# Kernel tuning notes

Hardware: AMD Instinct MI355X
Metric: run time of the kernel (lower is better)

## Reference

```python
import jax, jax.numpy as jnp
import numpy as np

B, C0, N, K = 8, 3, 2048, 20
EMB = 1024
NUM_CLASS = 40
EPS = 1e-5
SLOPE = 0.2


def setup_inputs() -> dict:
    key = jax.random.key(0)
    ks = jax.random.split(key, 16)
    rn = lambda k, s: jax.random.normal(k, s, jnp.float32) * 0.05
    inp = {
        'x': jax.random.normal(ks[0], (B, C0, N), jnp.float32),
        # 1x1 conv weights (out_ch, in_ch)
        'w1': rn(ks[1], (64, 6)),
        'w2': rn(ks[2], (64, 128)),
        'w3': rn(ks[3], (128, 128)),
        'w4': rn(ks[4], (256, 256)),
        'w5': rn(ks[5], (EMB, 512)),
        # linear layers
        'lw1': rn(ks[6], (512, 2 * EMB)),
        'lw2': rn(ks[7], (256, 512)),
        'lb2': jnp.zeros((256,), jnp.float32),
        'lw3': rn(ks[8], (NUM_CLASS, 256)),
        'lb3': jnp.zeros((NUM_CLASS,), jnp.float32),
    }
    # batchnorm affine params (bn1..bn7)
    for i, c in zip(range(1, 8), (64, 64, 128, 256, EMB, 512, 256)):
        inp['g%d' % i] = jnp.ones((c,), jnp.float32)
        inp['b%d' % i] = jnp.zeros((c,), jnp.float32)
    return inp


def lrelu(x):
    return jnp.where(x >= 0, x, SLOPE * x)


def bn(x, g, b, axes):
    # training-mode batchnorm over `axes`, channel axis = 1 (or last for 2D)
    m = jnp.mean(x, axis=axes, keepdims=True)
    v = jnp.var(x, axis=axes, keepdims=True)
    shp = [1] * x.ndim
    ch_ax = 1 if x.ndim > 1 else 0
    shp[ch_ax] = g.shape[0]
    return (x - m) * jax.lax.rsqrt(v + EPS) * g.reshape(shp) + b.reshape(shp)


def knn_idx(x, k):
    # x: [B, C, N]; topk of -||xi - xj||^2 -> k nearest (incl. self)
    inner = -2.0 * jnp.einsum('bcn,bcm->bnm', x, x)
    xx = jnp.sum(x * x, axis=1)  # [B, N]
    pd = -xx[:, :, None] - inner - xx[:, None, :]
    return jax.lax.top_k(pd, k)[1]  # [B, N, k]


def graph_feature(x, k):
    # x: [B, C, N] -> [B, 2C, N, k]
    b_, c_, n_ = x.shape
    idx = knn_idx(x, k)
    xt = jnp.transpose(x, (0, 2, 1))  # [B, N, C]
    nbr = xt[jnp.arange(b_)[:, None, None], idx]  # [B, N, k, C] irregular gather
    ctr = xt[:, :, None, :]
    feat = jnp.concatenate([nbr - ctr, jnp.broadcast_to(ctr, nbr.shape)], axis=-1)
    return jnp.transpose(feat, (0, 3, 1, 2))


def edge_block(x, w, g, b, k):
    f = graph_feature(x, k)                      # [B, 2C, N, k]
    y = jnp.einsum('oc,bcnk->bonk', w, f)        # 1x1 conv2d
    y = lrelu(bn(y, g, b, (0, 2, 3)))
    return jnp.max(y, axis=-1)                   # max over k -> [B, O, N]


def reference(x, w1, w2, w3, w4, w5, lw1, lw2, lb2, lw3, lb3,
              g1, b1, g2, b2, g3, b3, g4, b4, g5, b5, g6, b6, g7, b7):
    x1 = edge_block(x, w1, g1, b1, K)   # [B, 64, N]
    x2 = edge_block(x1, w2, g2, b2, K)  # [B, 64, N]
    x3 = edge_block(x2, w3, g3, b3, K)  # [B, 128, N]
    x4 = edge_block(x3, w4, g4, b4, K)  # [B, 256, N]
    cat = jnp.concatenate([x1, x2, x3, x4], axis=1)  # [B, 512, N]
    y = lrelu(bn(jnp.einsum('oc,bcn->bon', w5, cat), g5, b5, (0, 2)))  # [B, EMB, N]
    p = jnp.concatenate([jnp.max(y, axis=-1), jnp.mean(y, axis=-1)], axis=1)  # [B, 2*EMB]
    h = lrelu(bn(p @ lw1.T, g6, b6, (0,)))
    h = lrelu(bn(h @ lw2.T + lb2, g7, b7, (0,)))  # dropout = identity (eval)
    return h @ lw3.T + lb3  # [B, NUM_CLASS]
```

## Files before the change

### kernel.cpp

```cpp
#include <hip/hip_runtime.h>
#include <float.h>

constexpr int cB = 8;
constexpr int cN = 2048;
constexpr int cKnn = 20;
constexpr float F_EPS = 1e-5f;
constexpr float F_SLOPE = 0.2f;

__device__ __forceinline__ float lrelu(float x){ return x >= 0.f ? x : F_SLOPE * x; }

typedef __bf16 bf16x8 __attribute__((ext_vector_type(8)));
typedef float  f32x4  __attribute__((ext_vector_type(4)));
union U16x8 { uint4 u; bf16x8 v; };

__device__ __forceinline__ unsigned short f2bf(float x){
    unsigned u = __builtin_bit_cast(unsigned, x);
    unsigned r = u + 0x7FFFu + ((u >> 16) & 1u);
    return (unsigned short)(r >> 16);
}
__device__ __forceinline__ float bf2f(unsigned short h){
    return __builtin_bit_cast(float, (unsigned)h << 16);
}
__device__ __forceinline__ bf16x8 ldfrag(const unsigned short* p){
    U16x8 t; t.u = *(const uint4*)p; return t.v;
}
__device__ __forceinline__ unsigned f2key(float s){
    unsigned u = __builtin_bit_cast(unsigned, s);
    return (s >= 0.f) ? (u | 0x80000000u) : ~u;
}

__global__ void k_transpose3(const float* __restrict__ x, float* __restrict__ xt, float* __restrict__ xx){
    int i = blockIdx.x * 256 + threadIdx.x;
    if(i >= cB * cN) return;
    int b = i / cN, n = i % cN;
    const float* xb = x + (size_t)b * 3 * cN;
    float a = xb[n], c = xb[cN + n], d = xb[2*cN + n];
    float* o = xt + (size_t)i * 4;
    o[0] = a; o[1] = c; o[2] = d; o[3] = 0.f;
    xx[i] = a*a + c*c + d*d;
}

template<int Cin, int O, int CP>
__device__ __forceinline__ void prep_split_elem(const float* __restrict__ w, unsigned short* __restrict__ whl, int e){
    int c = e % CP, o2 = e / CP;
    float val = 0.f;
    if(c < Cin){
        if(o2 < O) val = w[o2 * 2 * Cin + c];
        else { int o = o2 - O; val = w[o * 2 * Cin + Cin + c] - w[o * 2 * Cin + c]; }
    }
    unsigned short h = f2bf(val);
    unsigned short l = f2bf(val - bf2f(h));
    whl[(size_t)o2 * 2 * CP + c] = h;
    whl[(size_t)o2 * 2 * CP + CP + c] = l;
}

__global__ void k_prepall(const float* __restrict__ w1, const float* __restrict__ w2,
                          const float* __restrict__ w3, const float* __restrict__ w4,
                          const float* __restrict__ w5,
                          float* __restrict__ ww, unsigned short* __restrict__ whl2,
                          unsigned short* __restrict__ whl3, unsigned short* __restrict__ whl4,
                          unsigned short* __restrict__ w5b){
    int e = blockIdx.x * 256 + threadIdx.x;
    if(e < 512){
        int op = e % 128, c = e / 128;
        float val = 0.f;
        if(c < 3){
            if(op < 64) val = w1[op * 6 + c];
            else { int o = op - 64; val = w1[o * 6 + 3 + c] - w1[o * 6 + c]; }
        }
        ww[e] = val;
        return;
    }
    e -= 512;
    if(e < 8192){ prep_split_elem<64, 64, 64>(w2, whl2, e); return; }
    e -= 8192;
    if(e < 16384){ prep_split_elem<64, 128, 64>(w3, whl3, e); return; }
    e -= 16384;
    if(e < 65536){ prep_split_elem<128, 256, 128>(w4, whl4, e); return; }
    e -= 65536;
    if(e < 524288) w5b[e] = f2bf(w5[e]);
}

template<int C>
__global__ __launch_bounds__(256) void k_score(const float* __restrict__ xt, const float* __restrict__ xx,
                                               float* __restrict__ S){
    __shared__ float at[16][68];
    __shared__ float bt[16][68];
    int tid = threadIdx.x;
    int j0 = blockIdx.x * 64, q0 = blockIdx.y * 64, b = blockIdx.z;
    const float* Xb = xt + (size_t)b * cN * C;
    int no = tid % 16, mo = tid / 16;
    float acc[4][4] = {};
    {
        if(tid < 64){
            float4 v = *(const float4*)(Xb + (size_t)(q0 + tid) * C);
            at[0][tid] = v.x; at[1][tid] = v.y; at[2][tid] = v.z; at[3][tid] = v.w;
            float4 w = *(const float4*)(Xb + (size_t)(j0 + tid) * C);
            bt[0][tid] = w.x; bt[1][tid] = w.y; bt[2][tid] = w.z; bt[3][tid] = w.w;
        }
        __syncthreads();
        #pragma unroll
        for(int c = 0; c < C; c++){
            float av[4] = { at[c][mo*4+0], at[c][mo*4+1], at[c][mo*4+2], at[c][mo*4+3] };
            float bv[4] = { bt[c][no*4+0], bt[c][no*4+1], bt[c][no*4+2], bt[c][no*4+3] };
            #pragma unroll
            for(int i2 = 0; i2 < 4; i2++)
                #pragma unroll
                for(int j2 = 0; j2 < 4; j2++)
                    acc[i2][j2] += av[i2] * bv[j2];
        }
    }
    const float* xxb = xx + (size_t)b * cN;
    float4 xv = *(const float4*)(xxb + j0 + no * 4);
    #pragma unroll
    for(int i2 = 0; i2 < 4; i2++){
        float4 o = make_float4(2.f*acc[i2][0] - xv.x, 2.f*acc[i2][1] - xv.y,
                               2.f*acc[i2][2] - xv.z, 2.f*acc[i2][3] - xv.w);
        *(float4*)(S + ((size_t)b * cN + q0 + mo * 4 + i2) * cN + j0 + no * 4) = o;
    }
}

template<int C>
__global__ __launch_bounds__(256) void k_score_mfma(const unsigned short* __restrict__ XHL,
                                                    const float* __restrict__ xx,
                                                    float* __restrict__ S){
    constexpr int SROW = 2 * C;
    constexpr int KST = C / 32;
    __shared__ unsigned short As[128 * 40];
    __shared__ unsigned short Bs[128 * 40];
    int tid = threadIdx.x;
    int lane = tid & 63, wave = tid >> 6;
    int wm = wave & 1, wn = wave >> 1;
    int q0 = blockIdx.y * 128, j0 = blockIdx.x * 128, b = blockIdx.z;
    const unsigned short* Xb = XHL + (size_t)b * cN * SROW;
    int m = lane & 15, quad = lane >> 4;
    f32x4 acc[4][4] = {};

    for(int seg = 0; seg < 3; seg++){
        int aoff = (seg == 2) ? C : 0;
        int boff = (seg == 1) ? C : 0;
        for(int kk = 0; kk < KST; kk++){
            __syncthreads();
            #pragma unroll
            for(int h = 0; h < 2; h++){
                int cidx = tid + h * 256;
                int row = cidx >> 2, cc = cidx & 3;
                *(uint4*)&As[row*40 + cc*8] = *(const uint4*)(Xb + (size_t)(q0 + row) * SROW + aoff + kk*32 + cc*8);
                *(uint4*)&Bs[row*40 + cc*8] = *(const uint4*)(Xb + (size_t)(j0 + row) * SROW + boff + kk*32 + cc*8);
            }
            __syncthreads();
            bf16x8 af[4], bfr[4];
            #pragma unroll
            for(int t = 0; t < 4; t++){
                af[t]  = ldfrag(&As[(wm*64 + t*16 + m)*40 + quad*8]);
                bfr[t] = ldfrag(&Bs[(wn*64 + t*16 + m)*40 + quad*8]);
            }
            #pragma unroll
            for(int i = 0; i < 4; i++)
                #pragma unroll
                for(int j = 0; j < 4; j++)
                    acc[i][j] = __builtin_amdgcn_mfma_f32_16x16x32_bf16(af[i], bfr[j], acc[i][j], 0, 0, 0);
        }
    }
    const float* xxb = xx + (size_t)b * cN;
    #pragma unroll
    for(int j = 0; j < 4; j++){
        int jj = j0 + wn*64 + j*16 + m;
        float xv = xxb[jj];
        #pragma unroll
        for(int i = 0; i < 4; i++){
            int r0 = q0 + wm*64 + i*16 + quad*4;
            #pragma unroll
            for(int r = 0; r < 4; r++)
                S[((size_t)b * cN + r0 + r) * cN + jj] = 2.f * acc[i][j][r] - xv;
        }
    }
}

__global__ __launch_bounds__(256) void k_select(const float* __restrict__ S, int* __restrict__ idxout){
    __shared__ unsigned skey[2][44];
    __shared__ int      sidx[2][44];
    int tid = threadIdx.x;
    int wave = tid >> 6, lane = tid & 63;
    int row = wave >> 1;
    int w   = wave & 1;
    int n = blockIdx.x * 2 + row;
    int b = blockIdx.y;
    const float* rowp = S + ((size_t)b * cN + n) * cN + w * 1024 + lane * 16;
    unsigned key[16];
    {
        const float4* rp4 = (const float4*)rowp;
        float4 v0 = rp4[0], v1 = rp4[1], v2 = rp4[2], v3 = rp4[3];
        key[0]=f2key(v0.x); key[1]=f2key(v0.y); key[2]=f2key(v0.z); key[3]=f2key(v0.w);
        key[4]=f2key(v1.x); key[5]=f2key(v1.y); key[6]=f2key(v1.z); key[7]=f2key(v1.w);
        key[8]=f2key(v2.x); key[9]=f2key(v2.y); key[10]=f2key(v2.z); key[11]=f2key(v2.w);
        key[12]=f2key(v3.x); key[13]=f2key(v3.y); key[14]=f2key(v3.z); key[15]=f2key(v3.w);
    }
    unsigned T = 0; bool exact = false;
    for(int bit = 31; bit >= 0; bit--){
        unsigned test = T | (1u << bit);
        int c = 0;
        #pragma unroll
        for(int i = 0; i < 16; i++) c += (key[i] >= test) ? 1 : 0;
        #pragma unroll
        for(int off = 32; off; off >>= 1) c += __shfl_xor(c, off);
        if(c >= cKnn){
            T = test;
            if(c == cKnn){ exact = true; break; }
        }
    }
    int jbase = w * 1024 + lane * 16;
    int pos = 0;
    if(exact){
        #pragma unroll
        for(int i = 0; i < 16; i++){
            bool hi = key[i] >= T;
            unsigned long long mm = __ballot(hi);
            if(hi){
                int r = __popcll(mm & ((1ull << lane) - 1ull));
                skey[row][w*20 + pos + r] = key[i];
                sidx[row][w*20 + pos + r] = jbase + i;
            }
            pos += __popcll(mm);
        }
    } else {
        int nab = 0;
        #pragma unroll
        for(int i = 0; i < 16; i++) nab += (key[i] > T) ? 1 : 0;
        #pragma unroll
        for(int off = 32; off; off >>= 1) nab += __shfl_xor(nab, off);
        int need = cKnn - nab;
        #pragma unroll
        for(int i = 0; i < 16; i++){
            bool hi = key[i] > T;
            unsigned long long mm = __ballot(hi);
            if(hi){
                int r = __popcll(mm & ((1ull << lane) - 1ull));
                skey[row][w*20 + pos + r] = key[i];
                sidx[row][w*20 + pos + r] = jbase + i;
            }
            pos += __popcll(mm);
        }
        for(int i = 0; i < 16 && need > 0; i++){
            bool eq = (key[i] == T);
            unsigned long long mm = __ballot(eq);
            int r = __popcll(mm & ((1ull << lane) - 1ull));
            if(eq && r < need){
                skey[row][w*20 + pos + r] = key[i];
                sidx[row][w*20 + pos + r] = jbase + i;
            }
            int t = __popcll(mm); t = t < need ? t : need;
            pos += t; need -= t;
        }
    }
    __syncthreads();
    if(w) return;
    unsigned k40 = (lane < 40) ? skey[row][lane] : 0u;
    int      j40 = (lane < 40) ? sidx[row][lane] : 0;
    unsigned Tg = 0; bool ex = false;
    for(int bit = 31; bit >= 0; bit--){
        unsigned test = Tg | (1u << bit);
        int c = __popcll(__ballot((lane < 40) && (k40 >= test)));
        if(c >= cKnn){
            Tg = test;
            if(c == cKnn){ ex = true; break; }
        }
    }
    int* out = idxout + ((size_t)b * cN + n) * cKnn;
    if(ex){
        bool hi = (lane < 40) && (k40 >= Tg);
        unsigned long long mm = __ballot(hi);
        if(hi){ int r = __popcll(mm & ((1ull << lane) - 1ull)); out[r] = j40; }
    } else {
        bool hi = (lane < 40) && (k40 > Tg);
        unsigned long long mm = __ballot(hi);
        if(hi){ int r = __popcll(mm & ((1ull << lane) - 1ull)); out[r] = j40; }
        int nab = __popcll(mm);
        int need = cKnn - nab;
        bool eq = (lane < 40) && (k40 == Tg);
        unsigned long long me = __ballot(eq);
        int r = __popcll(me & ((1ull << lane) - 1ull));
        if(eq && r < need) out[nab + r] = j40;
    }
}

template<int K, int W2O>
__global__ __launch_bounds__(256) void k_uw(const float* __restrict__ xt, const float* __restrict__ ww,
                                            float* __restrict__ UW){
    __shared__ float at[16][68];
    __shared__ float bt[16][68];
    int tid = threadIdx.x;
    int o0 = blockIdx.x * 64, q0 = blockIdx.y * 64, b = blockIdx.z;
    const float* Xb = xt + (size_t)b * cN * K;
    int no = tid % 16, mo = tid / 16;
    float acc[4][4] = {};
    {
        if(tid < 64){
            float4 v = *(const float4*)(Xb + (size_t)(q0 + tid) * K);
            at[0][tid] = v.x; at[1][tid] = v.y; at[2][tid] = v.z; at[3][tid] = v.w;
            int cc = tid >> 4, n4 = tid & 15;
            float4 wv = *(const float4*)(ww + (size_t)cc * W2O + o0 + n4 * 4);
            bt[cc][n4*4+0] = wv.x; bt[cc][n4*4+1] = wv.y;
            bt[cc][n4*4+2] = wv.z; bt[cc][n4*4+3] = wv.w;
        }
        __syncthreads();
        #pragma unroll
        for(int c = 0; c < K; c++){
            float av[4] = { at[c][mo*4+0], at[c][mo*4+1], at[c][mo*4+2], at[c][mo*4+3] };
            float bv[4] = { bt[c][no*4+0], bt[c][no*4+1], bt[c][no*4+2], bt[c][no*4+3] };
            #pragma unroll
            for(int i2 = 0; i2 < 4; i2++)
                #pragma unroll
                for(int j2 = 0; j2 < 4; j2++)
                    acc[i2][j2] += av[i2] * bv[j2];
        }
    }
    #pragma unroll
    for(int i2 = 0; i2 < 4; i2++){
        float4 v = make_float4(acc[i2][0], acc[i2][1], acc[i2][2], acc[i2][3]);
        *(float4*)(UW + ((size_t)b * cN + q0 + mo * 4 + i2) * W2O + o0 + no * 4) = v;
    }
}

template<int C, int W2O>
__global__ __launch_bounds__(256) void k_uw_mfma(const unsigned short* __restrict__ XHL,
                                                 const unsigned short* __restrict__ WHL,
                                                 float* __restrict__ UW){
    constexpr int SROW = 2 * C;
    constexpr int KST = C / 32;
    __shared__ unsigned short As[128 * 40];
    __shared__ unsigned short Bs[128 * 40];
    int tid = threadIdx.x;
    int lane = tid & 63, wave = tid >> 6;
    int wm = wave & 1, wn = wave >> 1;
    int n0 = blockIdx.x * 128, q0 = blockIdx.y * 128, b = blockIdx.z;
    const unsigned short* Xb = XHL + (size_t)b * cN * SROW;
    int m = lane & 15, quad = lane >> 4;
    f32x4 acc[4][4] = {};

    for(int seg = 0; seg < 3; seg++){
        int aoff = (seg == 2) ? C : 0;
        int boff = (seg == 1) ? C : 0;
        for(int kk = 0; kk < KST; kk++){
            __syncthreads();
            #pragma unroll
            for(int h = 0; h < 2; h++){
                int cidx = tid + h * 256;
                int row = cidx >> 2, cc = cidx & 3;
                *(uint4*)&As[row*40 + cc*8] = *(const uint4*)(Xb + (size_t)(q0 + row) * SROW + aoff + kk*32 + cc*8);
                *(uint4*)&Bs[row*40 + cc*8] = *(const uint4*)(WHL + (size_t)(n0 + row) * SROW + boff + kk*32 + cc*8);
            }
            __syncthreads();
            bf16x8 af[4], bfr[4];
            #pragma unroll
            for(int t = 0; t < 4; t++){
                af[t]  = ldfrag(&As[(wm*64 + t*16 + m)*40 + quad*8]);
                bfr[t] = ldfrag(&Bs[(wn*64 + t*16 + m)*40 + quad*8]);
            }
            #pragma unroll
            for(int i = 0; i < 4; i++)
                #pragma unroll
                for(int j = 0; j < 4; j++)
                    acc[i][j] = __builtin_amdgcn_mfma_f32_16x16x32_bf16(af[i], bfr[j], acc[i][j], 0, 0, 0);
        }
    }
    #pragma unroll
    for(int i = 0; i < 4; i++){
        int r0 = q0 + wm*64 + i*16 + quad*4;
        #pragma unroll
        for(int j = 0; j < 4; j++){
            int col = n0 + wn*64 + j*16 + m;
            #pragma unroll
            for(int r = 0; r < 4; r++)
                UW[((size_t)b * cN + r0 + r) * W2O + col] = acc[i][j][r];
        }
    }
}

template<int O>
__global__ __launch_bounds__(256) void k_gmax(const float* __restrict__ UW, const int* __restrict__ idx,
                                              float* __restrict__ Mbuf, float* __restrict__ bsum, float* __restrict__ bsq){
    constexpr int VEC = O / 64;
    constexpr int W2O = 2 * O;
    int id = blockIdx.x;
    int b = id & 7;
    int base = (id >> 3) * 16;
    int tid = threadIdx.x;
    int w = tid >> 6, l = tid & 63;
    const float* U = UW + (size_t)b * cN * W2O;
    float lsum[VEC] = {}, lsq[VEC] = {};
    for(int p = 0; p < 4; p++){
        int n = base + w * 4 + p;
        const int* ip = idx + ((size_t)b * cN + n) * cKnn;
        int jj[cKnn];
        #pragma unroll
        for(int k = 0; k < cKnn; k++) jj[k] = ip[k];
        float mx[VEC], su[VEC] = {}, s2[VEC] = {};
        #pragma unroll
        for(int v = 0; v < VEC; v++) mx[v] = -FLT_MAX;
        #pragma unroll
        for(int k = 0; k < cKnn; k++){
            const float* ur = U + (size_t)jj[k] * W2O + l * VEC;
            float uv[VEC];
            if constexpr (VEC == 4){ float4 t = *(const float4*)ur; uv[0]=t.x; uv[1]=t.y; uv[2]=t.z; uv[3]=t.w; }
            else if constexpr (VEC == 2){ float2 t = *(const float2*)ur; uv[0]=t.x; uv[1]=t.y; }
            else { uv[0] = *ur; }
            #pragma unroll
            for(int v = 0; v < VEC; v++){
                mx[v] = fmaxf(mx[v], uv[v]); su[v] += uv[v]; s2[v] += uv[v]*uv[v];
            }
        }
        const float* wr = U + (size_t)n * W2O + O + l * VEC;
        float w2[VEC];
        if constexpr (VEC == 4){ float4 t = *(const float4*)wr; w2[0]=t.x; w2[1]=t.y; w2[2]=t.z; w2[3]=t.w; }
        else if constexpr (VEC == 2){ float2 t = *(const float2*)wr; w2[0]=t.x; w2[1]=t.y; }
        else { w2[0] = *wr; }
        float* mp = Mbuf + ((size_t)b * cN + n) * O + l * VEC;
        if constexpr (VEC == 4){
            *(float4*)mp = make_float4(mx[0]+w2[0], mx[1]+w2[1], mx[2]+w2[2], mx[3]+w2[3]);
        } else if constexpr (VEC == 2){
            *(float2*)mp = make_float2(mx[0]+w2[0], mx[1]+w2[1]);
        } else {
            *mp = mx[0] + w2[0];
        }
        #pragma unroll
        for(int v = 0; v < VEC; v++){
            lsum[v] += su[v] + (float)cKnn * w2[v];
            lsq[v]  += s2[v] + 2.f * w2[v] * su[v] + (float)cKnn * w2[v] * w2[v];
        }
    }
    int bkt = id & 63;
    #pragma unroll
    for(int v = 0; v < VEC; v++){
        atomicAdd(&bsum[bkt * O + l * VEC + v], lsum[v]);
        atomicAdd(&bsq [bkt * O + l * VEC + v], lsq[v]);
    }
}

template<int O>
__global__ void k_redstats(const float* __restrict__ bsum, const float* __restrict__ bsq,
                           const float* __restrict__ g, const float* __restrict__ bb,
                           float2* __restrict__ stats, float invcnt){
    int o = threadIdx.x;
    if(o >= O) return;
    float s = 0.f, q = 0.f;
    for(int k = 0; k < 64; k++){ s += bsum[k * O + o]; q += bsq[k * O + o]; }
    float m = s * invcnt;
    float v = q * invcnt - m * m;
    float sc = g[o] * rsqrtf(v + F_EPS);
    stats[o] = make_float2(sc, bb[o] - m * sc);
}

template<int O, bool WXT>
__global__ void k_normf(const float* __restrict__ Mbuf, const float2* __restrict__ stats,
                        unsigned short* __restrict__ catb, unsigned short* __restrict__ xhl,
                        float* __restrict__ xx, int ooff){
    __shared__ float part[4];
    int tid = threadIdx.x;
    size_t i = (size_t)blockIdx.x * 256 + tid;
    int o = i % O;
    size_t bn = i / O;
    float2 st = stats[o];
    float y = lrelu(Mbuf[i] * st.x + st.y);
    catb[bn * 512 + ooff + o] = f2bf(y);
    if constexpr (WXT){
        unsigned short h = f2bf(y);
        unsigned short l = f2bf(y - bf2f(h));
        xhl[bn * 2 * O + o] = h;
        xhl[bn * 2 * O + O + o] = l;
        float s = y * y;
        #pragma unroll
        for(int off = 32; off; off >>= 1) s += __shfl_xor(s, off);
        if constexpr (O == 64){
            if((tid & 63) == 0) xx[bn] = s;
        } else {
            int wv = tid >> 6;
            if((tid & 63) == 0) part[wv] = s;
            __syncthreads();
            if((tid & 127) == 0) xx[bn] = part[wv] + part[wv + 1];
        }
    }
}

__global__ __launch_bounds__(256) void k_gemm_z_mfma(const unsigned short* __restrict__ W5B,
                                                     const unsigned short* __restrict__ CATB,
                                                     float* __restrict__ z){
    __shared__ unsigned short As[128 * 40];
    __shared__ unsigned short Bs[128 * 40];
    int tid = threadIdx.x;
    int lane = tid & 63, wave = tid >> 6;
    int wm = wave & 1, wn = wave >> 1;
    int n0 = blockIdx.x * 128, o0 = blockIdx.y * 128, b = blockIdx.z;
    const unsigned short* Cb = CATB + (size_t)b * cN * 512;
    int m = lane & 15, quad = lane >> 4;
    f32x4 acc[4][4] = {};

    for(int kk = 0; kk < 16; kk++){
        __syncthreads();
        #pragma unroll
        for(int h = 0; h < 2; h++){
            int cidx = tid + h * 256;
            int row = cidx >> 2, cc = cidx & 3;
            *(uint4*)&As[row*40 + cc*8] = *(const uint4*)(W5B + (size_t)(o0 + row) * 512 + kk*32 + cc*8);
            *(uint4*)&Bs[row*40 + cc*8] = *(const uint4*)(Cb  + (size_t)(n0 + row) * 512 + kk*32 + cc*8);
        }
        __syncthreads();
        bf16x8 af[4], bfr[4];
        #pragma unroll
        for(int t = 0; t < 4; t++){
            af[t]  = ldfrag(&As[(wm*64 + t*16 + m)*40 + quad*8]);
            bfr[t] = ldfrag(&Bs[(wn*64 + t*16 + m)*40 + quad*8]);
        }
        #pragma unroll
        for(int i = 0; i < 4; i++)
            #pragma unroll
            for(int j = 0; j < 4; j++)
                acc[i][j] = __builtin_amdgcn_mfma_f32_16x16x32_bf16(af[i], bfr[j], acc[i][j], 0, 0, 0);
    }
    #pragma unroll
    for(int i = 0; i < 4; i++){
        int r0 = o0 + wm*64 + i*16 + quad*4;
        #pragma unroll
        for(int j = 0; j < 4; j++){
            int col = n0 + wn*64 + j*16 + m;
            #pragma unroll
            for(int r = 0; r < 4; r++)
                z[((size_t)b * 1024 + r0 + r) * cN + col] = acc[i][j][r];
        }
    }
}

__global__ void k_zstats(const float* __restrict__ z, const float* __restrict__ g5,
                         const float* __restrict__ b5, float2* __restrict__ stats){
    int o = blockIdx.x;
    int tid = threadIdx.x;
    __shared__ float ss[256], sq[256];
    float s = 0.f, q = 0.f;
    for(int e = tid; e < cB * cN; e += 256){
        int b = e >> 11, n = e & 2047;
        float v = z[((size_t)b * 1024 + o) * cN + n];
        s += v; q += v * v;
    }
    ss[tid] = s; sq[tid] = q; __syncthreads();
    for(int st = 128; st; st >>= 1){
        if(tid < st){ ss[tid] += ss[tid + st]; sq[tid] += sq[tid + st]; }
        __syncthreads();
    }
    if(tid == 0){
        float m = ss[0] / (float)(cB * cN);
        float v = sq[0] / (float)(cB * cN) - m * m;
        float sc = g5[o] * rsqrtf(v + F_EPS);
        stats[o] = make_float2(sc, b5[o] - m * sc);
    }
}

__global__ void k_pool(const float* __restrict__ z, const float2* __restrict__ stats,
                       float* __restrict__ p){
    int o = blockIdx.x, b = blockIdx.y;
    int tid = threadIdx.x;
    float2 st = stats[o];
    const float* row = z + ((size_t)b * 1024 + o) * cN;
    float mx = -FLT_MAX, sm = 0.f;
    for(int n = tid; n < cN; n += 256){
        float y = lrelu(row[n] * st.x + st.y);
        mx = fmaxf(mx, y); sm += y;
    }
    __shared__ float smx[256], ssm[256];
    smx[tid] = mx; ssm[tid] = sm; __syncthreads();
    for(int st2 = 128; st2; st2 >>= 1){
        if(tid < st2){ smx[tid] = fmaxf(smx[tid], smx[tid + st2]); ssm[tid] += ssm[tid + st2]; }
        __syncthreads();
    }
    if(tid == 0){
        p[(size_t)b * 2048 + o] = smx[0];
        p[(size_t)b * 2048 + 1024 + o] = ssm[0] * (1.f / cN);
    }
}

__global__ void k_fc1(const float* __restrict__ p, const float* __restrict__ lw1,
                      const float* __restrict__ g6, const float* __restrict__ b6,
                      float* __restrict__ h1){
    int f = blockIdx.x;
    int tid = threadIdx.x;
    const float* wrow = lw1 + (size_t)f * 2048;
    float acc[cB] = {};
    for(int i = tid; i < 2048; i += 64){
        float wv = wrow[i];
        #pragma unroll
        for(int b = 0; b < cB; b++) acc[b] += p[(size_t)b * 2048 + i] * wv;
    }
    #pragma unroll
    for(int b = 0; b < cB; b++){
        float v = acc[b];
        for(int off = 32; off; off >>= 1) v += __shfl_down(v, off);
        acc[b] = v;
    }
    if(tid == 0){
        float m = 0.f;
        #pragma unroll
        for(int b = 0; b < cB; b++) m += acc[b];
        m *= (1.f / cB);
        float var = 0.f;
        #pragma unroll
        for(int b = 0; b < cB; b++){ float d = acc[b] - m; var += d * d; }
        var *= (1.f / cB);
        float sc = g6[f] * rsqrtf(var + F_EPS);
        float sh = b6[f] - m * sc;
        #pragma unroll
        for(int b = 0; b < cB; b++) h1[(size_t)b * 512 + f] = lrelu(acc[b] * sc + sh);
    }
}

__global__ void k_fc2(const float* __restrict__ h1, const float* __restrict__ lw2,
                      const float* __restrict__ lb2, const float* __restrict__ g7,
                      const float* __restrict__ b7, float* __restrict__ h2){
    int f = blockIdx.x;
    int tid = threadIdx.x;
    const float* wrow = lw2 + (size_t)f * 512;
    float acc[cB] = {};
    for(int i = tid; i < 512; i += 64){
        float wv = wrow[i];
        #pragma unroll
        for(int b = 0; b < cB; b++) acc[b] += h1[(size_t)b * 512 + i] * wv;
    }
    #pragma unroll
    for(int b = 0; b < cB; b++){
        float v = acc[b];
        for(int off = 32; off; off >>= 1) v += __shfl_down(v, off);
        acc[b] = v;
    }
    if(tid == 0){
        float bias = lb2[f];
        #pragma unroll
        for(int b = 0; b < cB; b++) acc[b] += bias;
        float m = 0.f;
        #pragma unroll
        for(int b = 0; b < cB; b++) m += acc[b];
        m *= (1.f / cB);
        float var = 0.f;
        #pragma unroll
        for(int b = 0; b < cB; b++){ float d = acc[b] - m; var += d * d; }
        var *= (1.f / cB);
        float sc = g7[f] * rsqrtf(var + F_EPS);
        float sh = b7[f] - m * sc;
        #pragma unroll
        for(int b = 0; b < cB; b++) h2[(size_t)b * 256 + f] = lrelu(acc[b] * sc + sh);
    }
}

__global__ void k_fc3(const float* __restrict__ h2, const float* __restrict__ lw3,
                      const float* __restrict__ lb3, float* __restrict__ out){
    int cls = blockIdx.x;
    int tid = threadIdx.x;
    const float* wrow = lw3 + (size_t)cls * 256;
    float acc[cB] = {};
    for(int i = tid; i < 256; i += 64){
        float wv = wrow[i];
        #pragma unroll
        for(int b = 0; b < cB; b++) acc[b] += h2[(size_t)b * 256 + i] * wv;
    }
    #pragma unroll
    for(int b = 0; b < cB; b++){
        float v = acc[b];
        for(int off = 32; off; off >>= 1) v += __shfl_down(v, off);
        acc[b] = v;
    }
    if(tid == 0){
        float bias = lb3[cls];
        #pragma unroll
        for(int b = 0; b < cB; b++) out[(size_t)b * 40 + cls] = acc[b] + bias;
    }
}

extern "C" void kernel_launch(void* const* d_in, const int* in_sizes, int n_in,
                              void* d_out, int out_size, void* d_ws, size_t ws_size,
                              hipStream_t stream){
    (void)in_sizes; (void)n_in; (void)out_size; (void)ws_size;
    const float* x   = (const float*)d_in[0];
    const float* w1  = (const float*)d_in[1];
    const float* w2  = (const float*)d_in[2];
    const float* w3  = (const float*)d_in[3];
    const float* w4  = (const float*)d_in[4];
    const float* w5  = (const float*)d_in[5];
    const float* lw1 = (const float*)d_in[6];
    const float* lw2 = (const float*)d_in[7];
    const float* lb2 = (const float*)d_in[8];
    const float* lw3 = (const float*)d_in[9];
    const float* lb3 = (const float*)d_in[10];
    const float* g1 = (const float*)d_in[11]; const float* b1 = (const float*)d_in[12];
    const float* g2 = (const float*)d_in[13]; const float* b2 = (const float*)d_in[14];
    const float* g3 = (const float*)d_in[15]; const float* b3 = (const float*)d_in[16];
    const float* g4 = (const float*)d_in[17]; const float* b4 = (const float*)d_in[18];
    const float* g5 = (const float*)d_in[19]; const float* b5 = (const float*)d_in[20];
    const float* g6 = (const float*)d_in[21]; const float* b6 = (const float*)d_in[22];
    const float* g7 = (const float*)d_in[23]; const float* b7 = (const float*)d_in[24];

    char* base = (char*)d_ws;
    size_t off = 0;
    auto alloc = [&](size_t bytes) -> char* {
        char* pp = base + off;
        off += (bytes + 255) & ~(size_t)255;
        return pp;
    };
    float*  SC   = (float*) alloc(sizeof(float) * (size_t)cB * cN * cN);
    float*  XT   = (float*) alloc(sizeof(float) * (size_t)cB * cN * 4);
    float*  Z    = (float*) alloc(sizeof(float) * (size_t)cB * 1024 * cN);
    float*  MB   = (float*) alloc(sizeof(float) * (size_t)cB * cN * 256);
    int*    IDX  = (int*)   alloc(sizeof(int)   * (size_t)cB * cN * cKnn);
    float*  XX   = (float*) alloc(sizeof(float) * (size_t)cB * cN);
    float*  BS   = (float*) alloc(sizeof(float) * 4 * 2 * 64 * 256);
    float2* STATS= (float2*)alloc(sizeof(float2) * 1024);
    float*  WW   = (float*) alloc(sizeof(float) * 4 * 128);
    unsigned short* WHL2 = (unsigned short*)alloc(sizeof(short) * 128 * 128);
    unsigned short* WHL3 = (unsigned short*)alloc(sizeof(short) * 256 * 128);
    unsigned short* WHL4 = (unsigned short*)alloc(sizeof(short) * 512 * 256);
    unsigned short* XHL  = (unsigned short*)alloc(sizeof(short) * (size_t)cB * cN * 256);
    unsigned short* CATB = (unsigned short*)alloc(sizeof(short) * (size_t)cB * cN * 512);
    unsigned short* W5B  = (unsigned short*)alloc(sizeof(short) * 1024 * 512);
    float*  P    = (float*) alloc(sizeof(float) * (size_t)cB * 2048);
    float*  H1   = (float*) alloc(sizeof(float) * (size_t)cB * 512);
    float*  H2   = (float*) alloc(sizeof(float) * (size_t)cB * 256);
    float*  UW   = Z;
    float* BSUM0 = BS + 0 * 2 * 16384, *BSQ0 = BSUM0 + 16384;
    float* BSUM1 = BS + 1 * 2 * 16384, *BSQ1 = BSUM1 + 16384;
    float* BSUM2 = BS + 2 * 2 * 16384, *BSQ2 = BSUM2 + 16384;
    float* BSUM3 = BS + 3 * 2 * 16384, *BSQ3 = BSUM3 + 16384;

    const float invcnt = 1.f / (float)(cB * cN * cKnn);
    dim3 sc1Grid(cN / 64, cN / 64, cB);
    dim3 scmGrid(cN / 128, cN / 128, cB);
    dim3 selGrid(cN / 2, cB);
    int gmBlocks = (cN / 16) * cB;

    k_transpose3<<<64, 256, 0, stream>>>(x, XT, XX);
    k_prepall<<<(614912 + 255) / 256, 256, 0, stream>>>(w1, w2, w3, w4, w5, WW, WHL2, WHL3, WHL4, W5B);
    hipMemsetAsync(BS, 0, sizeof(float) * 4 * 2 * 16384, stream);

    k_score<4><<<sc1Grid, 256, 0, stream>>>(XT, XX, SC);
    k_select<<<selGrid, 256, 0, stream>>>(SC, IDX);
    k_uw<4, 128><<<dim3(2, 32, cB), 256, 0, stream>>>(XT, WW, UW);
    k_gmax<64><<<gmBlocks, 256, 0, stream>>>(UW, IDX, MB, BSUM0, BSQ0);
    k_redstats<64><<<1, 256, 0, stream>>>(BSUM0, BSQ0, g1, b1, STATS, invcnt);
    k_normf<64, true><<<(cB * cN * 64) / 256, 256, 0, stream>>>(MB, STATS, CATB, XHL, XX, 0);

    k_score_mfma<64><<<scmGrid, 256, 0, stream>>>(XHL, XX, SC);
    k_select<<<selGrid, 256, 0, stream>>>(SC, IDX);
    k_uw_mfma<64, 128><<<dim3(1, 16, cB), 256, 0, stream>>>(XHL, WHL2, UW);
    k_gmax<64><<<gmBlocks, 256, 0, stream>>>(UW, IDX, MB, BSUM1, BSQ1);
    k_redstats<64><<<1, 256, 0, stream>>>(BSUM1, BSQ1, g2, b2, STATS, invcnt);
    k_normf<64, true><<<(cB * cN * 64) / 256, 256, 0, stream>>>(MB, STATS, CATB, XHL, XX, 64);

    k_score_mfma<64><<<scmGrid, 256, 0, stream>>>(XHL, XX, SC);
    k_select<<<selGrid, 256, 0, stream>>>(SC, IDX);
    k_uw_mfma<64, 256><<<dim3(2, 16, cB), 256, 0, stream>>>(XHL, WHL3, UW);
    k_gmax<128><<<gmBlocks, 256, 0, stream>>>(UW, IDX, MB, BSUM2, BSQ2);
    k_redstats<128><<<1, 256, 0, stream>>>(BSUM2, BSQ2, g3, b3, STATS, invcnt);
    k_normf<128, true><<<(cB * cN * 128) / 256, 256, 0, stream>>>(MB, STATS, CATB, XHL, XX, 128);

    k_score_mfma<128><<<scmGrid, 256, 0, stream>>>(XHL, XX, SC);
    k_select<<<selGrid, 256, 0, stream>>>(SC, IDX);
    k_uw_mfma<128, 512><<<dim3(4, 16, cB), 256, 0, stream>>>(XHL, WHL4, UW);
    k_gmax<256><<<gmBlocks, 256, 0, stream>>>(UW, IDX, MB, BSUM3, BSQ3);
    k_redstats<256><<<1, 256, 0, stream>>>(BSUM3, BSQ3, g4, b4, STATS, invcnt);
    k_normf<256, false><<<(cB * cN * 256) / 256, 256, 0, stream>>>(MB, STATS, CATB, nullptr, nullptr, 256);

    k_gemm_z_mfma<<<dim3(cN / 128, 1024 / 128, cB), 256, 0, stream>>>(W5B, CATB, Z);
    k_zstats<<<1024, 256, 0, stream>>>(Z, g5, b5, STATS);
    k_pool<<<dim3(1024, cB), 256, 0, stream>>>(Z, STATS, P);
    k_fc1<<<512, 64, 0, stream>>>(P, lw1, g6, b6, H1);
    k_fc2<<<256, 64, 0, stream>>>(H1, lw2, lb2, g7, b7, H2);
    k_fc3<<<40, 64, 0, stream>>>(H2, lw3, lb3, (float*)d_out);
}
```

Measured before the change: 740.0 us.

## Store kNN score matrix as 16-bit order keys with exact tie-break refinement

Result: slower. 811.9 us (+9.7%).

```diff
diff --git a/kernel.cpp b/kernel.cpp
--- a/kernel.cpp
+++ b/kernel.cpp
@@ -83,7 +83,7 @@
 
 template<int C>
 __global__ __launch_bounds__(256) void k_score(const float* __restrict__ xt, const float* __restrict__ xx,
-                                               float* __restrict__ S){
+                                               unsigned short* __restrict__ S16){
     __shared__ float at[16][68];
     __shared__ float bt[16][68];
     int tid = threadIdx.x;
@@ -114,16 +114,16 @@
     float4 xv = *(const float4*)(xxb + j0 + no * 4);
     #pragma unroll
     for(int i2 = 0; i2 < 4; i2++){
-        float4 o = make_float4(2.f*acc[i2][0] - xv.x, 2.f*acc[i2][1] - xv.y,
-                               2.f*acc[i2][2] - xv.z, 2.f*acc[i2][3] - xv.w);
-        *(float4*)(S + ((size_t)b * cN + q0 + mo * 4 + i2) * cN + j0 + no * 4) = o;
+        unsigned p0 = (f2key(2.f*acc[i2][0] - xv.x) >> 16) | ((f2key(2.f*acc[i2][1] - xv.y) >> 16) << 16);
+        unsigned p1 = (f2key(2.f*acc[i2][2] - xv.z) >> 16) | ((f2key(2.f*acc[i2][3] - xv.w) >> 16) << 16);
+        *(uint2*)(S16 + ((size_t)b * cN + q0 + mo * 4 + i2) * cN + j0 + no * 4) = make_uint2(p0, p1);
     }
 }
 
 template<int C>
 __global__ __launch_bounds__(256) void k_score_mfma(const unsigned short* __restrict__ XHL,
                                                     const float* __restrict__ xx,
-                                                    float* __restrict__ S){
+                                                    unsigned short* __restrict__ S16){
     constexpr int SROW = 2 * C;
     constexpr int KST = C / 32;
     __shared__ unsigned short As[128 * 40];
@@ -172,115 +172,170 @@
             int r0 = q0 + wm*64 + i*16 + quad*4;
             #pragma unroll
             for(int r = 0; r < 4; r++)
-                S[((size_t)b * cN + r0 + r) * cN + jj] = 2.f * acc[i][j][r] - xv;
-        }
-    }
-}
-
-__global__ __launch_bounds__(256) void k_select(const float* __restrict__ S, int* __restrict__ idxout){
-    __shared__ unsigned skey[2][44];
-    __shared__ int      sidx[2][44];
+                S16[((size_t)b * cN + r0 + r) * cN + jj] = (unsigned short)(f2key(2.f * acc[i][j][r] - xv) >> 16);
+        }
+    }
+}
+
+template<int C, bool FP32SRC>
+__global__ __launch_bounds__(256) void k_select16(const unsigned short* __restrict__ S16,
+                                                  const float* __restrict__ xt,
+                                                  const unsigned short* __restrict__ xhl,
+                                                  const float* __restrict__ xx,
+                                                  int* __restrict__ idxout){
+    constexpr int CAP = 52;
+    __shared__ unsigned short sk[2][2 * CAP];
+    __shared__ int            sj[2][2 * CAP];
+    __shared__ int            scnt[2][2];
     int tid = threadIdx.x;
     int wave = tid >> 6, lane = tid & 63;
-    int row = wave >> 1;
-    int w   = wave & 1;
+    int row = wave >> 1, w = wave & 1;
     int n = blockIdx.x * 2 + row;
     int b = blockIdx.y;
-    const float* rowp = S + ((size_t)b * cN + n) * cN + w * 1024 + lane * 16;
-    unsigned key[16];
+
+    const unsigned short* rp = S16 + ((size_t)b * cN + n) * cN + w * 1024 + lane * 16;
+    unsigned k16[16];
     {
-        const float4* rp4 = (const float4*)rowp;
-        float4 v0 = rp4[0], v1 = rp4[1], v2 = rp4[2], v3 = rp4[3];
-        key[0]=f2key(v0.x); key[1]=f2key(v0.y); key[2]=f2key(v0.z); key[3]=f2key(v0.w);
-        key[4]=f2key(v1.x); key[5]=f2key(v1.y); key[6]=f2key(v1.z); key[7]=f2key(v1.w);
-        key[8]=f2key(v2.x); key[9]=f2key(v2.y); key[10]=f2key(v2.z); key[11]=f2key(v2.w);
-        key[12]=f2key(v3.x); key[13]=f2key(v3.y); key[14]=f2key(v3.z); key[15]=f2key(v3.w);
+        uint4 v0 = *(const uint4*)rp;
+        uint4 v1 = *(const uint4*)(rp + 8);
+        const unsigned* p0 = (const unsigned*)&v0;
+        const unsigned* p1 = (const unsigned*)&v1;
+        #pragma unroll
+        for(int q = 0; q < 4; q++){
+            k16[q*2+0] = p0[q] & 0xFFFFu; k16[q*2+1] = p0[q] >> 16;
+            k16[8+q*2+0] = p1[q] & 0xFFFFu; k16[8+q*2+1] = p1[q] >> 16;
+        }
     }
     unsigned T = 0; bool exact = false;
-    for(int bit = 31; bit >= 0; bit--){
+    for(int bit = 15; bit >= 0; bit--){
         unsigned test = T | (1u << bit);
         int c = 0;
         #pragma unroll
-        for(int i = 0; i < 16; i++) c += (key[i] >= test) ? 1 : 0;
+        for(int i = 0; i < 16; i++) c += (k16[i] >= test) ? 1 : 0;
         #pragma unroll
         for(int off = 32; off; off >>= 1) c += __shfl_xor(c, off);
-        if(c >= cKnn){
-            T = test;
-            if(c == cKnn){ exact = true; break; }
-        }
-    }
-    int jbase = w * 1024 + lane * 16;
+        if(c >= cKnn){ T = test; if(c == cKnn){ exact = true; break; } }
+    }
+    int base = w * CAP;
     int pos = 0;
-    if(exact){
+    unsigned thrHi = exact ? T : (T + 1u);
+    #pragma unroll
+    for(int i = 0; i < 16; i++){
+        bool hi = (k16[i] >= thrHi);
+        unsigned long long mm = __ballot(hi);
+        if(hi){
+            int r = __popcll(mm & ((1ull << lane) - 1ull));
+            sk[row][base + pos + r] = (unsigned short)k16[i];
+            sj[row][base + pos + r] = w * 1024 + lane * 16 + i;
+        }
+        pos += __popcll(mm);
+    }
+    if(!exact){
         #pragma unroll
         for(int i = 0; i < 16; i++){
-            bool hi = key[i] >= T;
-            unsigned long long mm = __ballot(hi);
-            if(hi){
-                int r = __popcll(mm & ((1ull << lane) - 1ull));
-                skey[row][w*20 + pos + r] = key[i];
-                sidx[row][w*20 + pos + r] = jbase + i;
+            bool eq = (k16[i] == T);
+            unsigned long long mm = __ballot(eq);
+            int r = __popcll(mm & ((1ull << lane) - 1ull));
+            int slot = pos + r;
+            if(eq && slot < CAP){
+                sk[row][base + slot] = (unsigned short)T;
+                sj[row][base + slot] = w * 1024 + lane * 16 + i;
             }
             pos += __popcll(mm);
-        }
-    } else {
-        int nab = 0;
-        #pragma unroll
-        for(int i = 0; i < 16; i++) nab += (key[i] > T) ? 1 : 0;
-        #pragma unroll
-        for(int off = 32; off; off >>= 1) nab += __shfl_xor(nab, off);
-        int need = cKnn - nab;
-        #pragma unroll
-        for(int i = 0; i < 16; i++){
-            bool hi = key[i] > T;
-            unsigned long long mm = __ballot(hi);
-            if(hi){
-                int r = __popcll(mm & ((1ull << lane) - 1ull));
-                skey[row][w*20 + pos + r] = key[i];
-                sidx[row][w*20 + pos + r] = jbase + i;
-            }
-            pos += __popcll(mm);
-        }
-        for(int i = 0; i < 16 && need > 0; i++){
-            bool eq = (key[i] == T);
-            unsigned long long mm = __ballot(eq);
-            int r = __popcll(mm & ((1ull << lane) - 1ull));
-            if(eq && r < need){
-                skey[row][w*20 + pos + r] = key[i];
-                sidx[row][w*20 + pos + r] = jbase + i;
-            }
-            int t = __popcll(mm); t = t < need ? t : need;
-            pos += t; need -= t;
-        }
-    }
+            if(pos >= CAP){ pos = CAP; break; }
+        }
+    }
+    if(lane == 0) scnt[row][w] = pos;
     __syncthreads();
     if(w) return;
-    unsigned k40 = (lane < 40) ? skey[row][lane] : 0u;
-    int      j40 = (lane < 40) ? sidx[row][lane] : 0;
-    unsigned Tg = 0; bool ex = false;
-    for(int bit = 31; bit >= 0; bit--){
+
+    int c0 = scnt[row][0], c1 = scnt[row][1];
+    int nc = c0 + c1;
+    unsigned ck[2]; int cj[2];
+    #pragma unroll
+    for(int s = 0; s < 2; s++){
+        int id = lane + s * 64;
+        bool v = id < nc;
+        int src = (id < c0) ? id : (CAP + (id - c0));
+        ck[s] = v ? (unsigned)sk[row][src] : 0u;
+        cj[s] = v ? sj[row][src] : 0;
+    }
+    unsigned Tg = 0; bool exg = false;
+    for(int bit = 15; bit >= 0; bit--){
         unsigned test = Tg | (1u << bit);
-        int c = __popcll(__ballot((lane < 40) && (k40 >= test)));
-        if(c >= cKnn){
-            Tg = test;
-            if(c == cKnn){ ex = true; break; }
-        }
-    }
+        int c = 0;
+        #pragma unroll
+        for(int s = 0; s < 2; s++) c += (ck[s] >= test) ? 1 : 0;
+        #pragma unroll
+        for(int off = 32; off; off >>= 1) c += __shfl_xor(c, off);
+        if(c >= cKnn){ Tg = test; if(c == cKnn){ exg = true; break; } }
+    }
+    int nab = 0, ceq = 0;
+    #pragma unroll
+    for(int s = 0; s < 2; s++){ nab += (ck[s] > Tg) ? 1 : 0; ceq += (ck[s] == Tg) ? 1 : 0; }
+    #pragma unroll
+    for(int off = 32; off; off >>= 1){ nab += __shfl_xor(nab, off); ceq += __shfl_xor(ceq, off); }
+
     int* out = idxout + ((size_t)b * cN + n) * cKnn;
-    if(ex){
-        bool hi = (lane < 40) && (k40 >= Tg);
+    unsigned thr = exg ? Tg : (Tg + 1u);
+    int pos2 = 0;
+    #pragma unroll
+    for(int s = 0; s < 2; s++){
+        bool hi = (ck[s] >= thr);
         unsigned long long mm = __ballot(hi);
-        if(hi){ int r = __popcll(mm & ((1ull << lane) - 1ull)); out[r] = j40; }
-    } else {
-        bool hi = (lane < 40) && (k40 > Tg);
-        unsigned long long mm = __ballot(hi);
-        if(hi){ int r = __popcll(mm & ((1ull << lane) - 1ull)); out[r] = j40; }
-        int nab = __popcll(mm);
-        int need = cKnn - nab;
-        bool eq = (lane < 40) && (k40 == Tg);
-        unsigned long long me = __ballot(eq);
-        int r = __popcll(me & ((1ull << lane) - 1ull));
-        if(eq && r < need) out[nab + r] = j40;
+        if(hi){ int r = __popcll(mm & ((1ull << lane) - 1ull)); out[pos2 + r] = cj[s]; }
+        pos2 += __popcll(mm);
+    }
+    if(exg) return;
+    int need = cKnn - nab;
+    if(ceq == need){
+        #pragma unroll
+        for(int s = 0; s < 2; s++){
+            bool eq = (ck[s] == Tg);
+            unsigned long long mm = __ballot(eq);
+            if(eq){ int r = __popcll(mm & ((1ull << lane) - 1ull)); out[pos2 + r] = cj[s]; }
+            pos2 += __popcll(mm);
+        }
+        return;
+    }
+    float sc[2];
+    #pragma unroll
+    for(int s = 0; s < 2; s++){
+        sc[s] = -FLT_MAX;
+        if(ck[s] == Tg){
+            int j = cj[s];
+            float dot = 0.f;
+            if constexpr (FP32SRC){
+                const float* xq = xt + ((size_t)b * cN + n) * 4;
+                const float* xj = xt + ((size_t)b * cN + j) * 4;
+                #pragma unroll
+                for(int c2 = 0; c2 < 4; c2++) dot += xq[c2] * xj[c2];
+            } else {
+                const unsigned short* xq = xhl + ((size_t)b * cN + n) * (2 * C);
+                const unsigned short* xj = xhl + ((size_t)b * cN + j) * (2 * C);
+                for(int c2 = 0; c2 < C; c2++){
+                    float aq = bf2f(xq[c2]) + bf2f(xq[C + c2]);
+                    float aj = bf2f(xj[c2]) + bf2f(xj[C + c2]);
+                    dot += aq * aj;
+                }
+            }
+            sc[s] = 2.f * dot - xx[(size_t)b * cN + cj[s]];
+        }
+    }
+    for(int t = 0; t < need; t++){
+        float mv = sc[0]; int mid = lane;
+        if(sc[1] > mv){ mv = sc[1]; mid = lane | 64; }
+        #pragma unroll
+        for(int off = 32; off; off >>= 1){
+            float ov = __shfl_xor(mv, off);
+            int oid = __shfl_xor(mid, off);
+            if(ov > mv || (ov == mv && oid < mid)){ mv = ov; mid = oid; }
+        }
+        int wl = mid & 63, ws = mid >> 6;
+        if(lane == wl){
+            out[pos2 + t] = cj[ws];
+            sc[ws] = -FLT_MAX;
+        }
     }
 }
 
@@ -702,7 +757,7 @@
         off += (bytes + 255) & ~(size_t)255;
         return pp;
     };
-    float*  SC   = (float*) alloc(sizeof(float) * (size_t)cB * cN * cN);
+    unsigned short* SC16 = (unsigned short*)alloc(sizeof(short) * (size_t)cB * cN * cN);
     float*  XT   = (float*) alloc(sizeof(float) * (size_t)cB * cN * 4);
     float*  Z    = (float*) alloc(sizeof(float) * (size_t)cB * 1024 * cN);
     float*  MB   = (float*) alloc(sizeof(float) * (size_t)cB * cN * 256);
@@ -736,29 +791,29 @@
     k_prepall<<<(614912 + 255) / 256, 256, 0, stream>>>(w1, w2, w3, w4, w5, WW, WHL2, WHL3, WHL4, W5B);
     hipMemsetAsync(BS, 0, sizeof(float) * 4 * 2 * 16384, stream);
 
-    k_score<4><<<sc1Grid, 256, 0, stream>>>(XT, XX, SC);
-    k_select<<<selGrid, 256, 0, stream>>>(SC, IDX);
+    k_score<4><<<sc1Grid, 256, 0, stream>>>(XT, XX, SC16);
+    k_select16<4, true><<<selGrid, 256, 0, stream>>>(SC16, XT, nullptr, XX, IDX);
     k_uw<4, 128><<<dim3(2, 32, cB), 256, 0, stream>>>(XT, WW, UW);
     k_gmax<64><<<gmBlocks, 256, 0, stream>>>(UW, IDX, MB, BSUM0, BSQ0);
     k_redstats<64><<<1, 256, 0, stream>>>(BSUM0, BSQ0, g1, b1, STATS, invcnt);
     k_normf<64, true><<<(cB * cN * 64) / 256, 256, 0, stream>>>(MB, STATS, CATB, XHL, XX, 0);
 
-    k_score_mfma<64><<<scmGrid, 256, 0, stream>>>(XHL, XX, SC);
-    k_select<<<selGrid, 256, 0, stream>>>(SC, IDX);
+    k_score_mfma<64><<<scmGrid, 256, 0, stream>>>(XHL, XX, SC16);
+    k_select16<64, false><<<selGrid, 256, 0, stream>>>(SC16, nullptr, XHL, XX, IDX);
     k_uw_mfma<64, 128><<<dim3(1, 16, cB), 256, 0, stream>>>(XHL, WHL2, UW);
     k_gmax<64><<<gmBlocks, 256, 0, stream>>>(UW, IDX, MB, BSUM1, BSQ1);
     k_redstats<64><<<1, 256, 0, stream>>>(BSUM1, BSQ1, g2, b2, STATS, invcnt);
     k_normf<64, true><<<(cB * cN * 64) / 256, 256, 0, stream>>>(MB, STATS, CATB, XHL, XX, 64);
 
-    k_score_mfma<64><<<scmGrid, 256, 0, stream>>>(XHL, XX, SC);
-    k_select<<<selGrid, 256, 0, stream>>>(SC, IDX);
+    k_score_mfma<64><<<scmGrid, 256, 0, stream>>>(XHL, XX, SC16);
+    k_select16<64, false><<<selGrid, 256, 0, stream>>>(SC16, nullptr, XHL, XX, IDX);
     k_uw_mfma<64, 256><<<dim3(2, 16, cB), 256, 0, stream>>>(XHL, WHL3, UW);
     k_gmax<128><<<gmBlocks, 256, 0, stream>>>(UW, IDX, MB, BSUM2, BSQ2);
     k_redstats<128><<<1, 256, 0, stream>>>(BSUM2, BSQ2, g3, b3, STATS, invcnt);
     k_normf<128, true><<<(cB * cN * 128) / 256, 256, 0, stream>>>(MB, STATS, CATB, XHL, XX, 128);
 
-    k_score_mfma<128><<<scmGrid, 256, 0, stream>>>(XHL, XX, SC);
-    k_select<<<selGrid, 256, 0, stream>>>(SC, IDX);
+    k_score_mfma<128><<<scmGrid, 256, 0, stream>>>(XHL, XX, SC16);
+    k_select16<128, false><<<selGrid, 256, 0, stream>>>(SC16, nullptr, XHL, XX, IDX);
     k_uw_mfma<128, 512><<<dim3(4, 16, cB), 256, 0, stream>>>(XHL, WHL4, UW);
     k_gmax<256><<<gmBlocks, 256, 0, stream>>>(UW, IDX, MB, BSUM3, BSQ3);
     k_redstats<256><<<1, 256, 0, stream>>>(BSUM3, BSQ3, g4, b4, STATS, invcnt);
```
